# Kernel tuning notes

Hardware: AMD Instinct MI355X
Metric: run time of the kernel (lower is better)

## Reference

```python
import jax, jax.numpy as jnp
import numpy as np

WIN = (7, 7)
NUM_HEADS = 6
DIM = 192
NW = 64          # windows per image
BATCH = 64       # images
B_ = BATCH * NW  # 4096 window-batches
N = WIN[0] * WIN[1]  # 49


def _relative_position_index():
    ch, cw = np.arange(WIN[0]), np.arange(WIN[1])
    coords = np.stack(np.meshgrid(ch, cw, indexing='ij'))          # [2, Wh, Ww]
    cf = coords.reshape(2, -1)                                      # [2, N]
    rel = cf[:, :, None] - cf[:, None, :]                           # [2, N, N]
    rel = rel.transpose(1, 2, 0).astype(np.int64)                   # [N, N, 2]
    rel[:, :, 0] += WIN[0] - 1
    rel[:, :, 1] += WIN[1] - 1
    rel[:, :, 0] *= 2 * WIN[1] - 1
    return rel.sum(-1).astype(np.int32)                             # [N, N]


def setup_inputs() -> dict:
    key = jax.random.key(0)
    ks = jax.random.split(key, 8)
    x = jax.random.normal(ks[0], (B_, N, DIM), dtype=jnp.float32)
    # additive shift-window mask: 0 where allowed, -100 where disallowed
    u = jax.random.uniform(ks[1], (NW, N, N))
    attn_mask = jnp.where(u < 0.15, -100.0, 0.0).astype(jnp.float32)
    rpb_table = jax.random.normal(ks[2], ((2 * WIN[0] - 1) * (2 * WIN[1] - 1), NUM_HEADS), dtype=jnp.float32) * 0.02
    rel_index = jnp.asarray(_relative_position_index())
    std = 1.0 / np.sqrt(DIM)
    qkv_w = jax.random.normal(ks[3], (3 * DIM, DIM), dtype=jnp.float32) * std
    qkv_b = jax.random.normal(ks[4], (3 * DIM,), dtype=jnp.float32) * 0.02
    proj_w = jax.random.normal(ks[5], (DIM, DIM), dtype=jnp.float32) * std
    proj_b = jax.random.normal(ks[6], (DIM,), dtype=jnp.float32) * 0.02
    return {"x": x, "attn_mask": attn_mask, "rpb_table": rpb_table,
            "rel_index": rel_index, "qkv_w": qkv_w, "qkv_b": qkv_b,
            "proj_w": proj_w, "proj_b": proj_b}


def reference(x, attn_mask, rpb_table, rel_index, qkv_w, qkv_b, proj_w, proj_b):
    Bw, n, C = x.shape
    H = NUM_HEADS
    hd = C // H
    scale = hd ** -0.5
    # qkv projection: [Bw, N, 3, H, hd] -> (3, Bw, H, N, hd)
    qkv = (x @ qkv_w.T + qkv_b).reshape(Bw, n, 3, H, hd).transpose(2, 0, 3, 1, 4)
    q, k, v = qkv[0], qkv[1], qkv[2]
    # gathered relative position bias: [H, N, N]
    rel_bias = rpb_table[rel_index.reshape(-1)].reshape(n, n, H).transpose(2, 0, 1)
    # scores [Bw, H, N, N]
    attn = jnp.einsum('bhnd,bhmd->bhnm', q * scale, k) + rel_bias[None]
    nW = attn_mask.shape[0]
    attn = attn.reshape(Bw // nW, nW, H, n, n) + attn_mask[None, :, None]
    attn = jax.nn.softmax(attn.reshape(Bw, H, n, n), axis=-1)
    out = jnp.einsum('bhnm,bhmd->bhnd', attn, v)  # [Bw, H, N, hd]
    out = out.transpose(0, 2, 1, 3).reshape(Bw, n, C)
    return out @ proj_w.T + proj_b
```

## Files before the change

kernel.cpp:

```cpp
#include <hip/hip_runtime.h>
#include <stdint.h>

typedef unsigned short ushort_t;
typedef __attribute__((ext_vector_type(8))) short bf16x8;
typedef __attribute__((ext_vector_type(4))) float f32x4;
typedef __attribute__((ext_vector_type(4))) unsigned int u32x4;

#define NTOK 49
#define DIMC 192
#define NH 6
#define HD 32
#define SCALE 0.17677669529663687f
#define XS 200
#define VTS 72
#define PS 72
#define MS 66
#define RS 68

#define OFF_X    0
#define OFF_Q    25600
#define OFF_K    51200
#define OFF_VT   76800
#define OFF_P    104448
#define OFF_MASK 122880
#define OFF_RPB  139776
#define OFF_REL  145184
#define OFF_BQ   153888
#define OFF_BP   156192
#define SMEM_BYTES 156960

#define QKVW_N (576 * 192)
#define PROJW_N (192 * 192)
#define QKV_GRP (4 * 9 * 6 * 64)
#define PROJ_GRP (4 * 3 * 6 * 64)
#define WBF_BYTES ((QKVW_N + PROJW_N) * 2)
#define BIAS_FLOATS (64 * 6 * 4 * 4 * 4 * 16 * 4)
#define WS_NEED1 ((size_t)WBF_BYTES)
#define WS_NEED2 ((size_t)WBF_BYTES + (size_t)BIAS_FLOATS * 4)

__device__ __forceinline__ ushort_t f2bf(float f) {
    uint32_t x = __builtin_bit_cast(uint32_t, f);
    x += 0x7fffu + ((x >> 16) & 1u);
    return (ushort_t)(x >> 16);
}
__device__ __forceinline__ uint32_t cvtpk(float lo, float hi) {
    uint32_t r;
    asm("v_cvt_pk_bf16_f32 %0, %1, %2" : "=v"(r) : "v"(lo), "v"(hi));
    return r;
}

__device__ __forceinline__ bf16x8 cvt8(const float* p) {
    f32x4 a = *(const f32x4*)p;
    f32x4 b = *(const f32x4*)(p + 4);
    bf16x8 r;
    r[0] = (short)f2bf(a[0]); r[1] = (short)f2bf(a[1]);
    r[2] = (short)f2bf(a[2]); r[3] = (short)f2bf(a[3]);
    r[4] = (short)f2bf(b[0]); r[5] = (short)f2bf(b[1]);
    r[6] = (short)f2bf(b[2]); r[7] = (short)f2bf(b[3]);
    return r;
}

__global__ __launch_bounds__(256) void swz_weights_kernel(
    const float* __restrict__ qkvw, const float* __restrict__ projw,
    ushort_t* __restrict__ dst)
{
    int i = blockIdx.x * 256 + threadIdx.x;
    if (i >= QKV_GRP + PROJ_GRP) return;
    const float* src;
    float s = 1.0f;
    if (i < QKV_GRP) {
        int lane = i & 63, t = i >> 6;
        int kk = t % 6, nt = (t / 6) % 9, cq = t / 54;
        int col = cq * 144 + nt * 16 + (lane & 15);
        int k0 = kk * 32 + (lane >> 4) * 8;
        src = qkvw + col * DIMC + k0;
        if (col < 192) s = SCALE;
    } else {
        int j = i - QKV_GRP;
        int lane = j & 63, t = j >> 6;
        int kk = t % 6, nt = (t / 6) % 3, cq = t / 18;
        int col = cq * 48 + nt * 16 + (lane & 15);
        int k0 = kk * 32 + (lane >> 4) * 8;
        src = projw + col * DIMC + k0;
    }
    f32x4 a = *(const f32x4*)src;
    f32x4 b = *(const f32x4*)(src + 4);
    u32x4 o;
    o[0] = (uint32_t)f2bf(a[0] * s) | ((uint32_t)f2bf(a[1] * s) << 16);
    o[1] = (uint32_t)f2bf(a[2] * s) | ((uint32_t)f2bf(a[3] * s) << 16);
    o[2] = (uint32_t)f2bf(b[0] * s) | ((uint32_t)f2bf(b[1] * s) << 16);
    o[3] = (uint32_t)f2bf(b[2] * s) | ((uint32_t)f2bf(b[3] * s) << 16);
    *(u32x4*)(dst + (size_t)i * 8) = o;
}

__global__ __launch_bounds__(256) void bias_kernel(
    const float* __restrict__ mask_g, const float* __restrict__ rpb_g,
    const int* __restrict__ rel_g, float* __restrict__ dst)
{
    int i = blockIdx.x * 256 + threadIdx.x;
    if (i >= BIAS_FLOATS / 4) return;
    int c = i & 15, g = (i >> 4) & 3, t = (i >> 6) & 3, wsid = (i >> 8) & 3;
    int hw = i >> 10;
    int h = hw % 6, wi = hw / 6;
    int m0 = 16 * wsid + 4 * g, n = 16 * t + c;
    f32x4 v;
    #pragma unroll
    for (int r = 0; r < 4; ++r) {
        int m = m0 + r;
        float val;
        if (n >= NTOK)      val = -30000.0f;
        else if (m >= NTOK) val = 0.0f;
        else val = mask_g[(size_t)wi * (NTOK * NTOK) + m * NTOK + n]
                 + rpb_g[(size_t)rel_g[m * NTOK + n] * NH + h];
        v[r] = val;
    }
    *(f32x4*)(dst + (size_t)i * 4) = v;
}

template <int MODE>
__global__ __launch_bounds__(512, 2) void win_attn_kernel(
    const float* __restrict__ x_g,
    const float* __restrict__ mask_g,
    const float* __restrict__ rpb_g,
    const int* __restrict__ rel_g,
    const float* __restrict__ qkvw_g,
    const float* __restrict__ qkvb_g,
    const float* __restrict__ projw_g,
    const float* __restrict__ projb_g,
    const ushort_t* __restrict__ wbf_g,
    const float* __restrict__ bias_g,
    float* __restrict__ out_g)
{
    extern __shared__ char smem[];
    ushort_t* x_lds  = (ushort_t*)(smem + OFF_X);
    ushort_t* q_lds  = (ushort_t*)(smem + OFF_Q);
    ushort_t* k_lds  = (ushort_t*)(smem + OFF_K);
    ushort_t* vT     = (ushort_t*)(smem + OFF_VT);
    ushort_t* P_lds  = (ushort_t*)(smem + OFF_P);
    float*    mask_p = (float*)(smem + OFF_MASK);
    float*    rpb_l  = (float*)(smem + OFF_RPB);
    ushort_t* rel_p  = (ushort_t*)(smem + OFF_REL);
    float*    bq     = (float*)(smem + OFF_BQ);
    float*    bp     = (float*)(smem + OFF_BP);

    const int tid  = threadIdx.x;
    const int b    = blockIdx.x;
    const int wi   = b & 63;
    const int w    = tid >> 6;
    const int lane = tid & 63;
    const int g    = lane >> 4;
    const int c    = lane & 15;

    {
        const float* xg = x_g + (size_t)b * (NTOK * DIMC);
        for (int i = tid; i < 64 * 24; i += 512) {
            int row = i / 24, col = (i % 24) * 8;
            u32x4 v = {0u, 0u, 0u, 0u};
            if (row < NTOK) {
                const float* src = xg + row * DIMC + col;
                f32x4 a = *(const f32x4*)src;
                f32x4 d = *(const f32x4*)(src + 4);
                v[0] = cvtpk(a[0], a[1]); v[1] = cvtpk(a[2], a[3]);
                v[2] = cvtpk(d[0], d[1]); v[3] = cvtpk(d[2], d[3]);
            }
            *(u32x4*)&x_lds[row * XS + col] = v;
        }
        if constexpr (MODE < 2) {
            const float* mw = mask_g + (size_t)wi * (NTOK * NTOK);
            for (int i = tid; i < 64 * 64; i += 512) {
                int m = i >> 6, n = i & 63;
                float f;
                if (n >= NTOK)      f = -30000.0f;
                else if (m >= NTOK) f = 0.0f;
                else                f = mw[m * NTOK + n];
                mask_p[m * MS + n] = f;
                rel_p[m * RS + n] = (m < NTOK && n < NTOK) ? (ushort_t)rel_g[m * NTOK + n]
                                                           : (ushort_t)0;
            }
            for (int i = tid; i < 169 * 6; i += 512)
                rpb_l[(i / 6) * 8 + (i % 6)] = rpb_g[i];
        }
        for (int i = tid; i < 576; i += 512) {
            float v = qkvb_g[i];
            if constexpr (MODE >= 1) { if (i < 192) v *= SCALE; }
            bq[i] = v;
        }
        if (tid < 192) bp[tid] = projb_g[tid];
    }
    __syncthreads();

    {
        const int mh = w >> 2, cq = w & 3;
        const ushort_t* wq = wbf_g + (size_t)cq * (9 * 6 * 64 * 8);

        bf16x8 ring[4][6];
        if constexpr (MODE >= 1) {
            #pragma unroll
            for (int p = 0; p < 3; ++p)
                #pragma unroll
                for (int kk = 0; kk < 6; ++kk)
                    ring[p][kk] = *(const bf16x8*)(wq + (size_t)((p * 6 + kk) * 64 + lane) * 8);
            __builtin_amdgcn_sched_barrier(0);
        }

        bf16x8 ax[2][6];
        #pragma unroll
        for (int mt = 0; mt < 2; ++mt)
            #pragma unroll
            for (int kk = 0; kk < 6; ++kk)
                ax[mt][kk] = *(const bf16x8*)&x_lds[(32 * mh + 16 * mt + c) * XS + kk * 32 + g * 8];

        #pragma unroll
        for (int nt = 0; nt < 9; ++nt) {
            const int cg = 144 * cq + nt * 16 + c;
            bf16x8 bw[6];
            if constexpr (MODE >= 1) {
                if (nt + 3 < 9) {
                    #pragma unroll
                    for (int kk = 0; kk < 6; ++kk)
                        ring[(nt + 3) & 3][kk] =
                            *(const bf16x8*)(wq + (size_t)(((nt + 3) * 6 + kk) * 64 + lane) * 8);
                }
                __builtin_amdgcn_sched_barrier(0);
                #pragma unroll
                for (int kk = 0; kk < 6; ++kk) bw[kk] = ring[nt & 3][kk];
            } else {
                #pragma unroll
                for (int kk = 0; kk < 6; ++kk)
                    bw[kk] = cvt8(qkvw_g + (size_t)cg * DIMC + kk * 32 + g * 8);
            }
            const float bias = bq[cg];
            f32x4 acc[2];
            acc[0] = (f32x4){bias, bias, bias, bias};
            acc[1] = acc[0];
            #pragma unroll
            for (int kk = 0; kk < 6; ++kk)
                #pragma unroll
                for (int mt = 0; mt < 2; ++mt)
                    acc[mt] = __builtin_amdgcn_mfma_f32_16x16x32_bf16(ax[mt][kk], bw[kk], acc[mt], 0, 0, 0);

            const int seg = 144 * cq + nt * 16;
            if (seg < 192) {
                #pragma unroll
                for (int mt = 0; mt < 2; ++mt) {
                    uint32_t p01 = cvtpk(acc[mt][0], acc[mt][1]);
                    uint32_t p23 = cvtpk(acc[mt][2], acc[mt][3]);
                    const int r0 = 32 * mh + 16 * mt + g * 4;
                    q_lds[(r0 + 0) * XS + cg] = (ushort_t)p01;
                    q_lds[(r0 + 1) * XS + cg] = (ushort_t)(p01 >> 16);
                    q_lds[(r0 + 2) * XS + cg] = (ushort_t)p23;
                    q_lds[(r0 + 3) * XS + cg] = (ushort_t)(p23 >> 16);
                }
            } else if (seg < 384) {
                const int ck = cg - 192;
                #pragma unroll
                for (int mt = 0; mt < 2; ++mt) {
                    uint32_t p01 = cvtpk(acc[mt][0], acc[mt][1]);
                    uint32_t p23 = cvtpk(acc[mt][2], acc[mt][3]);
                    const int r0 = 32 * mh + 16 * mt + g * 4;
                    k_lds[(r0 + 0) * XS + ck] = (ushort_t)p01;
                    k_lds[(r0 + 1) * XS + ck] = (ushort_t)(p01 >> 16);
                    k_lds[(r0 + 2) * XS + ck] = (ushort_t)p23;
                    k_lds[(r0 + 3) * XS + ck] = (ushort_t)(p23 >> 16);
                }
            } else {
                const int cv = cg - 384;
                #pragma unroll
                for (int mt = 0; mt < 2; ++mt) {
                    uint32_t* dst = (uint32_t*)&vT[cv * VTS + 32 * mh + 16 * mt + g * 4];
                    dst[0] = cvtpk(acc[mt][0], acc[mt][1]);
                    dst[1] = cvtpk(acc[mt][2], acc[mt][3]);
                }
            }
        }
    }
    __syncthreads();

    bf16x8 pw[3][6];
    {
        const int wsid = w & 3, hh = w >> 2;
        ushort_t* Pw = P_lds + w * (16 * PS);
        const int mq0 = 16 * wsid + g * 4;

        if constexpr (MODE == 2) {
            const int h0 = hh * 3;
            float rinv0[4], rinv1[4], rinv2[4];
            f32x4 S0[4], S1[4], S2[4];

            auto QKT = [&](int h, f32x4* S) {
                bf16x8 aq = *(const bf16x8*)&q_lds[(16 * wsid + c) * XS + h * HD + g * 8];
                const float* bC = bias_g + ((size_t)((wi * 6 + h) * 4 + wsid) * 4) * 256 + lane * 4;
                __builtin_amdgcn_s_setprio(1);
                #pragma unroll
                for (int t = 0; t < 4; ++t) {
                    f32x4 Ct = *(const f32x4*)(bC + t * 256);
                    bf16x8 bk = *(const bf16x8*)&k_lds[(16 * t + c) * XS + h * HD + g * 8];
                    S[t] = __builtin_amdgcn_mfma_f32_16x16x32_bf16(aq, bk, Ct, 0, 0, 0);
                }
                __builtin_amdgcn_s_setprio(0);
            };
            auto SM = [&](f32x4* S, float* rinv) {
                #pragma unroll
                for (int r = 0; r < 4; ++r) {
                    float e0 = __expf(S[0][r]), e1 = __expf(S[1][r]);
                    float e2 = __expf(S[2][r]), e3 = __expf(S[3][r]);
                    float sum = (e0 + e1) + (e2 + e3);
                    #pragma unroll
                    for (int xm = 1; xm < 16; xm <<= 1)
                        sum += __shfl_xor(sum, xm);
                    rinv[r] = 1.0f / sum;
                    uint32_t p01 = cvtpk(e0, e1);
                    uint32_t p23 = cvtpk(e2, e3);
                    ushort_t* pr = Pw + (g * 4 + r) * PS + c;
                    pr[0]  = (ushort_t)p01;
                    pr[16] = (ushort_t)(p01 >> 16);
                    pr[32] = (ushort_t)p23;
                    pr[48] = (ushort_t)(p23 >> 16);
                }
            };
            auto PV = [&](int h, const float* rinv) {
                f32x4 z = {0.f, 0.f, 0.f, 0.f};
                f32x4 O[2] = {z, z};
                __builtin_amdgcn_s_setprio(1);
                #pragma unroll
                for (int ks = 0; ks < 2; ++ks) {
                    bf16x8 ap = *(const bf16x8*)&Pw[c * PS + ks * 32 + g * 8];
                    #pragma unroll
                    for (int nt = 0; nt < 2; ++nt) {
                        bf16x8 bv = *(const bf16x8*)&vT[(h * HD + nt * 16 + c) * VTS + ks * 32 + g * 8];
                        O[nt] = __builtin_amdgcn_mfma_f32_16x16x32_bf16(ap, bv, O[nt], 0, 0, 0);
                    }
                }
                __builtin_amdgcn_s_setprio(0);
                #pragma unroll
                for (int r = 0; r < 4; ++r) {
                    uint32_t po = cvtpk(O[0][r] * rinv[r], O[1][r] * rinv[r]);
                    ushort_t* ar = x_lds + (16 * wsid + g * 4 + r) * XS + h * HD + c;
                    ar[0]  = (ushort_t)po;
                    ar[16] = (ushort_t)(po >> 16);
                }
            };

            QKT(h0 + 0, S0);
            QKT(h0 + 1, S1);
            SM(S0, rinv0);
            QKT(h0 + 2, S2);
            PV(h0 + 0, rinv0);
            SM(S1, rinv1);
            PV(h0 + 1, rinv1);
            {
                const int cq4 = w & 3;
                const ushort_t* wp = wbf_g + QKVW_N + (size_t)cq4 * (3 * 6 * 64 * 8);
                #pragma unroll
                for (int nt = 0; nt < 3; ++nt)
                    #pragma unroll
                    for (int kk = 0; kk < 6; ++kk)
                        pw[nt][kk] = *(const bf16x8*)(wp + (size_t)((nt * 6 + kk) * 64 + lane) * 8);
                __builtin_amdgcn_sched_barrier(0);
            }
            SM(S2, rinv2);
            PV(h0 + 2, rinv2);
        } else {
            auto head = [&](int h) {
                bf16x8 aq = *(const bf16x8*)&q_lds[(16 * wsid + c) * XS + h * HD + g * 8];
                f32x4 S[4];
                #pragma unroll
                for (int t = 0; t < 4; ++t) {
                    bf16x8 bk = *(const bf16x8*)&k_lds[(16 * t + c) * XS + h * HD + g * 8];
                    f32x4 z = {0.f, 0.f, 0.f, 0.f};
                    S[t] = __builtin_amdgcn_mfma_f32_16x16x32_bf16(aq, bk, z, 0, 0, 0);
                }
                float rinv[4];
                #pragma unroll
                for (int r = 0; r < 4; ++r) {
                    const int mq = mq0 + r;
                    const float*    mrow = mask_p + mq * MS;
                    const ushort_t* rrow = rel_p + mq * RS;
                    float sv[4];
                    #pragma unroll
                    for (int t = 0; t < 4; ++t) {
                        const int n = 16 * t + c;
                        float sc = (MODE == 0) ? SCALE : 1.0f;
                        sv[t] = S[t][r] * sc + rpb_l[(int)rrow[n] * 8 + h] + mrow[n];
                    }
                    float vmax = fmaxf(fmaxf(sv[0], sv[1]), fmaxf(sv[2], sv[3]));
                    #pragma unroll
                    for (int xm = 1; xm < 16; xm <<= 1)
                        vmax = fmaxf(vmax, __shfl_xor(vmax, xm));
                    float sum = 0.f;
                    float ev[4];
                    #pragma unroll
                    for (int t = 0; t < 4; ++t) {
                        ev[t] = __expf(fmaxf(sv[t] - vmax, -80.0f));
                        sum += ev[t];
                    }
                    #pragma unroll
                    for (int xm = 1; xm < 16; xm <<= 1)
                        sum += __shfl_xor(sum, xm);
                    rinv[r] = 1.0f / sum;
                    uint32_t p01 = cvtpk(ev[0], ev[1]);
                    uint32_t p23 = cvtpk(ev[2], ev[3]);
                    ushort_t* pr = Pw + (g * 4 + r) * PS + c;
                    pr[0]  = (ushort_t)p01;
                    pr[16] = (ushort_t)(p01 >> 16);
                    pr[32] = (ushort_t)p23;
                    pr[48] = (ushort_t)(p23 >> 16);
                }
                f32x4 z = {0.f, 0.f, 0.f, 0.f};
                f32x4 O[2] = {z, z};
                #pragma unroll
                for (int ks = 0; ks < 2; ++ks) {
                    bf16x8 ap = *(const bf16x8*)&Pw[c * PS + ks * 32 + g * 8];
                    #pragma unroll
                    for (int nt = 0; nt < 2; ++nt) {
                        bf16x8 bv = *(const bf16x8*)&vT[(h * HD + nt * 16 + c) * VTS + ks * 32 + g * 8];
                        O[nt] = __builtin_amdgcn_mfma_f32_16x16x32_bf16(ap, bv, O[nt], 0, 0, 0);
                    }
                }
                #pragma unroll
                for (int r = 0; r < 4; ++r) {
                    uint32_t po = cvtpk(O[0][r] * rinv[r], O[1][r] * rinv[r]);
                    ushort_t* ar = x_lds + (16 * wsid + g * 4 + r) * XS + h * HD + c;
                    ar[0]  = (ushort_t)po;
                    ar[16] = (ushort_t)(po >> 16);
                }
            };
            head(hh * 3 + 0);
            head(hh * 3 + 1);
            if constexpr (MODE >= 1) {
                const int cq4 = w & 3;
                const ushort_t* wp = wbf_g + QKVW_N + (size_t)cq4 * (3 * 6 * 64 * 8);
                #pragma unroll
                for (int nt = 0; nt < 3; ++nt)
                    #pragma unroll
                    for (int kk = 0; kk < 6; ++kk)
                        pw[nt][kk] = *(const bf16x8*)(wp + (size_t)((nt * 6 + kk) * 64 + lane) * 8);
                __builtin_amdgcn_sched_barrier(0);
            }
            head(hh * 3 + 2);
        }
    }
    __syncthreads();

    {
        const int mh = w >> 2, cq4 = w & 3;
        bf16x8 aa[2][6];
        #pragma unroll
        for (int mt = 0; mt < 2; ++mt)
            #pragma unroll
            for (int kk = 0; kk < 6; ++kk)
                aa[mt][kk] = *(const bf16x8*)&x_lds[(32 * mh + 16 * mt + c) * XS + kk * 32 + g * 8];

        float* og = out_g + (size_t)b * (NTOK * DIMC);
        #pragma unroll
        for (int nt = 0; nt < 3; ++nt) {
            const int cg = 48 * cq4 + nt * 16 + c;
            bf16x8 bw[6];
            #pragma unroll
            for (int kk = 0; kk < 6; ++kk) {
                if constexpr (MODE >= 1)
                    bw[kk] = pw[nt][kk];
                else
                    bw[kk] = cvt8(projw_g + (size_t)cg * DIMC + kk * 32 + g * 8);
            }
            const float bias = bp[cg];
            f32x4 acc[2];
            acc[0] = (f32x4){bias, bias, bias, bias};
            acc[1] = acc[0];
            #pragma unroll
            for (int kk = 0; kk < 6; ++kk)
                #pragma unroll
                for (int mt = 0; mt < 2; ++mt)
                    acc[mt] = __builtin_amdgcn_mfma_f32_16x16x32_bf16(aa[mt][kk], bw[kk], acc[mt], 0, 0, 0);
            #pragma unroll
            for (int mt = 0; mt < 2; ++mt)
                #pragma unroll
                for (int r = 0; r < 4; ++r) {
                    const int row = 32 * mh + 16 * mt + g * 4 + r;
                    if (row < NTOK) og[row * DIMC + cg] = acc[mt][r];
                }
        }
    }
}

extern "C" void kernel_launch(void* const* d_in, const int* in_sizes, int n_in,
                              void* d_out, int out_size, void* d_ws, size_t ws_size,
                              hipStream_t stream) {
    (void)in_sizes; (void)n_in; (void)out_size;
    const float* x_g     = (const float*)d_in[0];
    const float* mask_g  = (const float*)d_in[1];
    const float* rpb_g   = (const float*)d_in[2];
    const int*   rel_g   = (const int*)d_in[3];
    const float* qkvw_g  = (const float*)d_in[4];
    const float* qkvb_g  = (const float*)d_in[5];
    const float* projw_g = (const float*)d_in[6];
    const float* projb_g = (const float*)d_in[7];
    float*       out_g   = (float*)d_out;

    const bool has_w = (d_ws != nullptr) && (ws_size >= WS_NEED1);
    const bool has_b = (d_ws != nullptr) && (ws_size >= WS_NEED2);
    ushort_t* wbf = (ushort_t*)d_ws;
    float* bias4 = (float*)((char*)d_ws + WBF_BYTES);

    if (has_w) {
        int ngrp = QKV_GRP + PROJ_GRP;
        hipLaunchKernelGGL(swz_weights_kernel, dim3((ngrp + 255) / 256), dim3(256), 0, stream,
                           qkvw_g, projw_g, wbf);
    }
    if (has_b) {
        int nthr = BIAS_FLOATS / 4;
        hipLaunchKernelGGL(bias_kernel, dim3((nthr + 255) / 256), dim3(256), 0, stream,
                           mask_g, rpb_g, rel_g, bias4);
        hipFuncSetAttribute((const void*)win_attn_kernel<2>,
                            hipFuncAttributeMaxDynamicSharedMemorySize, SMEM_BYTES);
        hipLaunchKernelGGL(win_attn_kernel<2>, dim3(4096), dim3(512), SMEM_BYTES, stream,
                           x_g, mask_g, rpb_g, rel_g, qkvw_g, qkvb_g, projw_g, projb_g,
                           wbf, bias4, out_g);
    } else if (has_w) {
        hipFuncSetAttribute((const void*)win_attn_kernel<1>,
                            hipFuncAttributeMaxDynamicSharedMemorySize, SMEM_BYTES);
        hipLaunchKernelGGL(win_attn_kernel<1>, dim3(4096), dim3(512), SMEM_BYTES, stream,
                           x_g, mask_g, rpb_g, rel_g, qkvw_g, qkvb_g, projw_g, projb_g,
                           wbf, (const float*)nullptr, out_g);
    } else {
        hipFuncSetAttribute((const void*)win_attn_kernel<0>,
                            hipFuncAttributeMaxDynamicSharedMemorySize, SMEM_BYTES);
        hipLaunchKernelGGL(win_attn_kernel<0>, dim3(4096), dim3(512), SMEM_BYTES, stream,
                           x_g, mask_g, rpb_g, rel_g, qkvw_g, qkvb_g, projw_g, projb_g,
                           (const ushort_t*)nullptr, (const float*)nullptr, out_g);
    }
}
```

Measured before the change: 221.3 us.

## Fold log2e into Q and bias, compute softmax row sums via MFMA

Pre-scales the Q weights, Q bias and the precomputed mask+bias by log2(e) so the MODE 2 softmax can call exp2f directly. The row-sum shuffle reductions are removed and the denominators are instead produced by an extra MFMA of P against a ones vector inside the PV loop. The prefetch of the first QKV weight ring is also hoisted before the x/mask staging so its global loads overlap with LDS fills. The trade is one more MFMA per k-step, and row sums now come from bf16-rounded probabilities, so normalisation accuracy changes slightly. Because the non-MODE-2 path still receives log2e-scaled Q, its scale is changed to LN2 to compensate.

```diff
diff --git a/kernel.cpp b/kernel.cpp
--- a/kernel.cpp
+++ b/kernel.cpp
@@ -1,5 +1,6 @@
 #include <hip/hip_runtime.h>
 #include <stdint.h>
+#include <cmath>
 
 typedef unsigned short ushort_t;
 typedef __attribute__((ext_vector_type(8))) short bf16x8;
@@ -11,6 +12,8 @@
 #define NH 6
 #define HD 32
 #define SCALE 0.17677669529663687f
+#define LOG2E 1.4426950408889634f
+#define LN2   0.6931471805599453f
 #define XS 200
 #define VTS 72
 #define PS 72
@@ -74,7 +77,7 @@
         int col = cq * 144 + nt * 16 + (lane & 15);
         int k0 = kk * 32 + (lane >> 4) * 8;
         src = qkvw + col * DIMC + k0;
-        if (col < 192) s = SCALE;
+        if (col < 192) s = SCALE * LOG2E;
     } else {
         int j = i - QKV_GRP;
         int lane = j & 63, t = j >> 6;
@@ -112,7 +115,7 @@
         else if (m >= NTOK) val = 0.0f;
         else val = mask_g[(size_t)wi * (NTOK * NTOK) + m * NTOK + n]
                  + rpb_g[(size_t)rel_g[m * NTOK + n] * NH + h];
-        v[r] = val;
+        v[r] = val * LOG2E;
     }
     *(f32x4*)(dst + (size_t)i * 4) = v;
 }
@@ -151,6 +154,20 @@
     const int g    = lane >> 4;
     const int c    = lane & 15;
 
+    bf16x8 ring[4][6];
+    {
+        if constexpr (MODE >= 1) {
+            const int cq = w & 3;
+            const ushort_t* wq = wbf_g + (size_t)cq * (9 * 6 * 64 * 8);
+            #pragma unroll
+            for (int p = 0; p < 3; ++p)
+                #pragma unroll
+                for (int kk = 0; kk < 6; ++kk)
+                    ring[p][kk] = *(const bf16x8*)(wq + (size_t)((p * 6 + kk) * 64 + lane) * 8);
+            __builtin_amdgcn_sched_barrier(0);
+        }
+    }
+
     {
         const float* xg = x_g + (size_t)b * (NTOK * DIMC);
         for (int i = tid; i < 64 * 24; i += 512) {
@@ -182,7 +199,7 @@
         }
         for (int i = tid; i < 576; i += 512) {
             float v = qkvb_g[i];
-            if constexpr (MODE >= 1) { if (i < 192) v *= SCALE; }
+            if constexpr (MODE >= 1) { if (i < 192) v *= SCALE * LOG2E; }
             bq[i] = v;
         }
         if (tid < 192) bp[tid] = projb_g[tid];
@@ -192,16 +209,6 @@
     {
         const int mh = w >> 2, cq = w & 3;
         const ushort_t* wq = wbf_g + (size_t)cq * (9 * 6 * 64 * 8);
-
-        bf16x8 ring[4][6];
-        if constexpr (MODE >= 1) {
-            #pragma unroll
-            for (int p = 0; p < 3; ++p)
-                #pragma unroll
-                for (int kk = 0; kk < 6; ++kk)
-                    ring[p][kk] = *(const bf16x8*)(wq + (size_t)((p * 6 + kk) * 64 + lane) * 8);
-            __builtin_amdgcn_sched_barrier(0);
-        }
 
         bf16x8 ax[2][6];
         #pragma unroll
@@ -284,8 +291,9 @@
 
         if constexpr (MODE == 2) {
             const int h0 = hh * 3;
-            float rinv0[4], rinv1[4], rinv2[4];
             f32x4 S0[4], S1[4], S2[4];
+            const short oneb = (short)0x3F80;
+            bf16x8 ones8 = {oneb, oneb, oneb, oneb, oneb, oneb, oneb, oneb};
 
             auto QKT = [&](int h, f32x4* S) {
                 bf16x8 aq = *(const bf16x8*)&q_lds[(16 * wsid + c) * XS + h * HD + g * 8];
@@ -299,16 +307,11 @@
                 }
                 __builtin_amdgcn_s_setprio(0);
             };
-            auto SM = [&](f32x4* S, float* rinv) {
+            auto SM = [&](f32x4* S) {
                 #pragma unroll
                 for (int r = 0; r < 4; ++r) {
-                    float e0 = __expf(S[0][r]), e1 = __expf(S[1][r]);
-                    float e2 = __expf(S[2][r]), e3 = __expf(S[3][r]);
-                    float sum = (e0 + e1) + (e2 + e3);
-                    #pragma unroll
-                    for (int xm = 1; xm < 16; xm <<= 1)
-                        sum += __shfl_xor(sum, xm);
-                    rinv[r] = 1.0f / sum;
+                    float e0 = exp2f(S[0][r]), e1 = exp2f(S[1][r]);
+                    float e2 = exp2f(S[2][r]), e3 = exp2f(S[3][r]);
                     uint32_t p01 = cvtpk(e0, e1);
                     uint32_t p23 = cvtpk(e2, e3);
                     ushort_t* pr = Pw + (g * 4 + r) * PS + c;
@@ -318,9 +321,10 @@
                     pr[48] = (ushort_t)(p23 >> 16);
                 }
             };
-            auto PV = [&](int h, const float* rinv) {
+            auto PV = [&](int h) {
                 f32x4 z = {0.f, 0.f, 0.f, 0.f};
                 f32x4 O[2] = {z, z};
+                f32x4 Osum = z;
                 __builtin_amdgcn_s_setprio(1);
                 #pragma unroll
                 for (int ks = 0; ks < 2; ++ks) {
@@ -330,11 +334,13 @@
                         bf16x8 bv = *(const bf16x8*)&vT[(h * HD + nt * 16 + c) * VTS + ks * 32 + g * 8];
                         O[nt] = __builtin_amdgcn_mfma_f32_16x16x32_bf16(ap, bv, O[nt], 0, 0, 0);
                     }
+                    Osum = __builtin_amdgcn_mfma_f32_16x16x32_bf16(ap, ones8, Osum, 0, 0, 0);
                 }
                 __builtin_amdgcn_s_setprio(0);
                 #pragma unroll
                 for (int r = 0; r < 4; ++r) {
-                    uint32_t po = cvtpk(O[0][r] * rinv[r], O[1][r] * rinv[r]);
+                    float rinv = 1.0f / Osum[r];
+                    uint32_t po = cvtpk(O[0][r] * rinv, O[1][r] * rinv);
                     ushort_t* ar = x_lds + (16 * wsid + g * 4 + r) * XS + h * HD + c;
                     ar[0]  = (ushort_t)po;
                     ar[16] = (ushort_t)(po >> 16);
@@ -343,11 +349,11 @@
 
             QKT(h0 + 0, S0);
             QKT(h0 + 1, S1);
-            SM(S0, rinv0);
+            SM(S0);
             QKT(h0 + 2, S2);
-            PV(h0 + 0, rinv0);
-            SM(S1, rinv1);
-            PV(h0 + 1, rinv1);
+            PV(h0 + 0);
+            SM(S1);
+            PV(h0 + 1);
             {
                 const int cq4 = w & 3;
                 const ushort_t* wp = wbf_g + QKVW_N + (size_t)cq4 * (3 * 6 * 64 * 8);
@@ -358,8 +364,8 @@
                         pw[nt][kk] = *(const bf16x8*)(wp + (size_t)((nt * 6 + kk) * 64 + lane) * 8);
                 __builtin_amdgcn_sched_barrier(0);
             }
-            SM(S2, rinv2);
-            PV(h0 + 2, rinv2);
+            SM(S2);
+            PV(h0 + 2);
         } else {
             auto head = [&](int h) {
                 bf16x8 aq = *(const bf16x8*)&q_lds[(16 * wsid + c) * XS + h * HD + g * 8];
@@ -380,7 +386,7 @@
                     #pragma unroll
                     for (int t = 0; t < 4; ++t) {
                         const int n = 16 * t + c;
-                        float sc = (MODE == 0) ? SCALE : 1.0f;
+                        float sc = (MODE == 0) ? SCALE : LN2;
                         sv[t] = S[t][r] * sc + rpb_l[(int)rrow[n] * 8 + h] + mrow[n];
                     }
                     float vmax = fmaxf(fmaxf(sv[0], sv[1]), fmaxf(sv[2], sv[3]));
```

Result: faster. 205.7 us (median of 3 runs) (-7.0%).
